# Kernel tuning notes

Measured on AMD Instinct MI355X. Metric: run time of the kernel, lower is better.

## Reference

```python
import jax, jax.numpy as jnp
import numpy as np

DIM = 256
HEADS = 8
HEAD_DIM = DIM // HEADS


def setup_inputs() -> dict:
    key = jax.random.key(0)
    ks = jax.random.split(key, 10)
    B, Nq, Nk, C = 2, 2048, 2048, DIM
    inp = {
        "query": jax.random.normal(ks[0], (B, Nq, C), jnp.float32),
        "key": jax.random.normal(ks[1], (B, Nk, C), jnp.float32),
        "value": jax.random.normal(ks[2], (B, Nk, C), jnp.float32),
        "qpos": jnp.zeros((B, Nq), jnp.int32),
        "kpos": jnp.zeros((B, Nk), jnp.int32),
        "mask": jax.random.randint(ks[3], (Nq, Nk), 0, 2) > 0,
        "similarities": jax.random.normal(ks[4], (B, HEADS, Nq, Nk), jnp.float32),
        # learned params (torch Linear stored here as [C_in, C_out]; no qkv bias)
        "Wq": jax.random.normal(ks[5], (C, C), jnp.float32) / np.sqrt(C),
        "Wk": jax.random.normal(ks[6], (C, C), jnp.float32) / np.sqrt(C),
        "Wv": jax.random.normal(ks[7], (C, C), jnp.float32) / np.sqrt(C),
        "Wp": jax.random.normal(ks[8], (C, C), jnp.float32) / np.sqrt(C),
        "bp": jax.random.normal(ks[9], (C,), jnp.float32) * 0.01,
    }
    return inp


def reference(query, key, value, qpos, kpos, mask, similarities, Wq, Wk, Wv, Wp, bp):
    B, Nq, C = query.shape
    Nk = key.shape[1]
    H, hd = HEADS, HEAD_DIM
    scale = hd ** -0.5
    # projections -> [B, N, H, hd] (rope is None, so qpos/kpos are unused)
    q = (query @ Wq).reshape(B, Nq, H, hd)
    k = (key @ Wk).reshape(B, Nk, H, hd)
    v = (value @ Wv).reshape(B, Nk, H, hd)
    # scores [B, H, Nq, Nk]
    attn = jnp.einsum("bqhd,bkhd->bhqk", q, k) * scale
    # mean-centered similarity bias (mean over heads, dim=1)
    attn = attn + (similarities - similarities.mean(axis=1, keepdims=True))
    # boolean mask: fill False positions with -inf, then softmax over keys
    attn = jnp.where(mask[None, None, :, :], attn, -jnp.inf)
    attn = jax.nn.softmax(attn, axis=-1)
    # AV -> [B, Nq, C], output projection
    x = jnp.einsum("bhqk,bkhd->bqhd", attn, v).reshape(B, Nq, C)
    return x @ Wp + bp
```

## Files before the change

kernel.cpp:

```cpp
#include <hip/hip_runtime.h>

#define B_  2
#define NQ  2048
#define NK  2048
#define C_  256
#define H_  8
#define HD  32
#define SPLIT 4
#define KSEG (NK / SPLIT)
#define KT   (KSEG / 32)
#define QT_  (NQ / 16)
#define PART_STRIDE 544

typedef float f32x4 __attribute__((ext_vector_type(4)));
typedef __bf16 bf16x8 __attribute__((ext_vector_type(8)));
typedef unsigned short ushort8 __attribute__((ext_vector_type(8)));

static __device__ __forceinline__ unsigned short f2bf(float f) {
    unsigned int u = __builtin_bit_cast(unsigned int, f);
    u += 0x7FFFu + ((u >> 16) & 1u);
    return (unsigned short)(u >> 16);
}
static __device__ __forceinline__ float bf2f(unsigned short h) {
    unsigned int u = ((unsigned int)h) << 16;
    return __builtin_bit_cast(float, u);
}
static __device__ __forceinline__ unsigned int split1(float f) {
    unsigned short h = f2bf(f);
    unsigned short l = f2bf(f - bf2f(h));
    return (unsigned int)h | ((unsigned int)l << 16);
}
static __device__ __forceinline__ bf16x8 ld_bf16x8(const unsigned short* p) {
    return __builtin_bit_cast(bf16x8, *(const ushort8*)p);
}
static __device__ __forceinline__ void async16(const void* g, void* l) {
    __builtin_amdgcn_global_load_lds((__attribute__((address_space(1))) void*)g,
                                     (__attribute__((address_space(3))) void*)l,
                                     16, 0, 0);
}

__global__ __launch_bounds__(256) void proj_kernel(
        const float* __restrict__ query, const float* __restrict__ key,
        const float* __restrict__ value,
        const float* __restrict__ Wq, const float* __restrict__ Wk,
        const float* __restrict__ Wv,
        unsigned short* __restrict__ qbh, unsigned short* __restrict__ qbl,
        unsigned short* __restrict__ kbh, unsigned short* __restrict__ kbl,
        unsigned short* __restrict__ vbh, unsigned short* __restrict__ vbl)
{
    __shared__ unsigned short WtH[64][32];
    __shared__ unsigned short WtL[64][32];

    const int z = blockIdx.z;
    const float* X = (z == 0) ? query : (z == 1) ? key : value;
    const float* W = (z == 0) ? Wq    : (z == 1) ? Wk  : Wv;
    unsigned short* dh = (z == 0) ? qbh : (z == 1) ? kbh : vbh;
    unsigned short* dl = (z == 0) ? qbl : (z == 1) ? kbl : vbl;
    const int vmode = (z == 2);

    const int tid  = threadIdx.x;
    const int wave = tid >> 6;
    const int lane = tid & 63;
    const int n15  = lane & 15;
    const int quad = lane >> 4;
    const int m0   = blockIdx.x * 64;
    const int j0   = blockIdx.y * 64;

    f32x4 acc[4];
    acc[0] = 0.f; acc[1] = 0.f; acc[2] = 0.f; acc[3] = 0.f;

    const int sj  = tid >> 2;
    const int skc = (tid & 3) * 8;
    const float* __restrict__ xrow = X + (size_t)(m0 + wave * 16 + n15) * C_;

    for (int k0 = 0; k0 < C_; k0 += 32) {
        ushort8 wh, wl;
        #pragma unroll
        for (int i = 0; i < 8; ++i) {
            unsigned int p = split1(W[(size_t)(k0 + skc + i) * C_ + j0 + sj]);
            wh[i] = (unsigned short)p;
            wl[i] = (unsigned short)(p >> 16);
        }
        *(ushort8*)&WtH[sj][skc] = wh;
        *(ushort8*)&WtL[sj][skc] = wl;
        __syncthreads();

        f32x4 a0 = *(const f32x4*)(xrow + k0 + quad * 8);
        f32x4 a1 = *(const f32x4*)(xrow + k0 + quad * 8 + 4);
        ushort8 ah, al;
        #pragma unroll
        for (int i = 0; i < 4; ++i) {
            unsigned int p0 = split1(a0[i]);
            unsigned int p1 = split1(a1[i]);
            ah[i]     = (unsigned short)p0;  al[i]     = (unsigned short)(p0 >> 16);
            ah[i + 4] = (unsigned short)p1;  al[i + 4] = (unsigned short)(p1 >> 16);
        }
        bf16x8 Ah = __builtin_bit_cast(bf16x8, ah);
        bf16x8 Al = __builtin_bit_cast(bf16x8, al);

        #pragma unroll
        for (int f = 0; f < 4; ++f) {
            bf16x8 Bh = ld_bf16x8(&WtH[f * 16 + n15][quad * 8]);
            bf16x8 Bl = ld_bf16x8(&WtL[f * 16 + n15][quad * 8]);
            acc[f] = __builtin_amdgcn_mfma_f32_16x16x32_bf16(Al, Bl, acc[f], 0, 0, 0);
            acc[f] = __builtin_amdgcn_mfma_f32_16x16x32_bf16(Al, Bh, acc[f], 0, 0, 0);
            acc[f] = __builtin_amdgcn_mfma_f32_16x16x32_bf16(Ah, Bl, acc[f], 0, 0, 0);
            acc[f] = __builtin_amdgcn_mfma_f32_16x16x32_bf16(Ah, Bh, acc[f], 0, 0, 0);
        }
        __syncthreads();
    }

    #pragma unroll
    for (int f = 0; f < 4; ++f) {
        const int j = j0 + f * 16 + n15;
        const int h = j >> 5, dd = j & 31;
        #pragma unroll
        for (int r = 0; r < 4; ++r) {
            const int grow = m0 + wave * 16 + quad * 4 + r;
            const int b = grow >> 11, row = grow & 2047;
            unsigned int p = split1(acc[f][r]);
            size_t idx;
            if (vmode) idx = (size_t)((b * H_ + h) * HD + dd) * NK + row;
            else       idx = (size_t)((b * H_ + h) * NK + row) * HD + dd;
            dh[idx] = (unsigned short)p;
            dl[idx] = (unsigned short)(p >> 16);
        }
    }
}

__global__ __launch_bounds__(256) void outproj_kernel(const unsigned short* __restrict__ Xh,
                                                      const unsigned short* __restrict__ Xl,
                                                      const float* __restrict__ W,
                                                      const float* __restrict__ bias,
                                                      float* __restrict__ out)
{
    __shared__ unsigned short WtH[64][32];
    __shared__ unsigned short WtL[64][32];

    const int tid  = threadIdx.x;
    const int wave = tid >> 6;
    const int lane = tid & 63;
    const int n15  = lane & 15;
    const int quad = lane >> 4;
    const int m0   = blockIdx.x * 64;
    const int j0   = blockIdx.y * 64;

    f32x4 acc[4];
    acc[0] = 0.f; acc[1] = 0.f; acc[2] = 0.f; acc[3] = 0.f;

    const int sj  = tid >> 2;
    const int skc = (tid & 3) * 8;
    const size_t xoff = (size_t)(m0 + wave * 16 + n15) * C_;

    for (int k0 = 0; k0 < C_; k0 += 32) {
        ushort8 wh, wl;
        #pragma unroll
        for (int i = 0; i < 8; ++i) {
            unsigned int p = split1(W[(size_t)(k0 + skc + i) * C_ + j0 + sj]);
            wh[i] = (unsigned short)p;
            wl[i] = (unsigned short)(p >> 16);
        }
        *(ushort8*)&WtH[sj][skc] = wh;
        *(ushort8*)&WtL[sj][skc] = wl;
        __syncthreads();

        bf16x8 Ah = ld_bf16x8(Xh + xoff + k0 + quad * 8);
        bf16x8 Al = ld_bf16x8(Xl + xoff + k0 + quad * 8);

        #pragma unroll
        for (int f = 0; f < 4; ++f) {
            bf16x8 Bh = ld_bf16x8(&WtH[f * 16 + n15][quad * 8]);
            bf16x8 Bl = ld_bf16x8(&WtL[f * 16 + n15][quad * 8]);
            acc[f] = __builtin_amdgcn_mfma_f32_16x16x32_bf16(Al, Bl, acc[f], 0, 0, 0);
            acc[f] = __builtin_amdgcn_mfma_f32_16x16x32_bf16(Al, Bh, acc[f], 0, 0, 0);
            acc[f] = __builtin_amdgcn_mfma_f32_16x16x32_bf16(Ah, Bl, acc[f], 0, 0, 0);
            acc[f] = __builtin_amdgcn_mfma_f32_16x16x32_bf16(Ah, Bh, acc[f], 0, 0, 0);
        }
        __syncthreads();
    }

    #pragma unroll
    for (int f = 0; f < 4; ++f) {
        const int j = j0 + f * 16 + n15;
        const float bj = bias[j];
        #pragma unroll
        for (int r = 0; r < 4; ++r) {
            const int grow = m0 + wave * 16 + quad * 4 + r;
            out[(size_t)grow * C_ + j] = acc[f][r] + bj;
        }
    }
}

__global__ __launch_bounds__(512, 6) void attn_kernel(
        const unsigned short* __restrict__ qh, const unsigned short* __restrict__ ql,
        const unsigned short* __restrict__ kh, const unsigned short* __restrict__ kl,
        const unsigned short* __restrict__ vh, const unsigned short* __restrict__ vl,
        const float* __restrict__ sim, const int* __restrict__ mask,
        float* __restrict__ part)
{
    __shared__ float simLds[2][H_][16][32];
    __shared__ int   maskLds[2][16][32];
    __shared__ float biasLds[16][33];
    __shared__ __align__(16) unsigned short pLds[H_][16 * 40];

    const int tid  = threadIdx.x;
    const int wave = tid >> 6;
    const int lane = tid & 63;
    const int n15  = lane & 15;
    const int quad = lane >> 4;

    const int wg   = blockIdx.x;
    const int s    = wg >> 8;
    const int rem  = wg & 255;
    const int b    = rem >> 7;
    const int qt   = rem & 127;
    const int q0   = qt * 16;
    const int kbeg = s * KSEG;

    const size_t bh   = (size_t)(b * H_ + wave);
    const size_t qoff = (bh * NQ + q0 + n15) * HD + quad * 8;
    const unsigned short* khb = kh + bh * NK * HD;
    const unsigned short* klb = kl + bh * NK * HD;
    const unsigned short* vhb = vh + bh * HD * NK;
    const unsigned short* vlb = vl + bh * HD * NK;
    const float* gsim = sim + (bh * NQ + q0) * (size_t)NK + kbeg
                            + (size_t)(lane >> 3) * NK + (lane & 7) * 4;
    const int* gmask = mask + (size_t)(q0 + (lane >> 3)) * NK + kbeg + (lane & 7) * 4;

    const bf16x8 Qh = ld_bf16x8(qh + qoff);
    const bf16x8 Ql = ld_bf16x8(ql + qoff);

    f32x4 O0 = 0.f, O1 = 0.f;
    float m_r[4] = {0.f, 0.f, 0.f, 0.f};
    float l_r[4] = {0.f, 0.f, 0.f, 0.f};

    async16(gsim,                  &simLds[0][wave][0][0]);
    async16(gsim + (size_t)8 * NK, &simLds[0][wave][8][0]);
    if (wave == 0) {
        async16(gmask,                  &maskLds[0][0][0]);
        async16(gmask + (size_t)8 * NK, &maskLds[0][8][0]);
    }

    const float scale = 0.17677669529663687f;

    for (int it = 0; it < KT; ++it) {
        const int k0  = kbeg + it * 32;
        const int cur = it & 1;

        __syncthreads();

        {
            const int qq = tid >> 5, kk = tid & 31;
            float sum = 0.f;
            #pragma unroll
            for (int h = 0; h < H_; ++h) sum += simLds[cur][h][qq][kk];
            biasLds[qq][kk] = maskLds[cur][qq][kk] ? (-0.125f * sum) : -1e30f;
        }
        __syncthreads();

        if (it + 1 < KT) {
            const float* g  = gsim + it * 32 + 32;
            async16(g,                  &simLds[cur ^ 1][wave][0][0]);
            async16(g + (size_t)8 * NK, &simLds[cur ^ 1][wave][8][0]);
            if (wave == 0) {
                const int* gm = gmask + it * 32 + 32;
                async16(gm,                  &maskLds[cur ^ 1][0][0]);
                async16(gm + (size_t)8 * NK, &maskLds[cur ^ 1][8][0]);
            }
        }

        const size_t koA = (size_t)(k0 + n15) * HD + quad * 8;
        const size_t koB = (size_t)(k0 + 16 + n15) * HD + quad * 8;
        bf16x8 Kh0 = ld_bf16x8(khb + koA), Kl0 = ld_bf16x8(klb + koA);
        bf16x8 Kh1 = ld_bf16x8(khb + koB), Kl1 = ld_bf16x8(klb + koB);

        f32x4 S0 = 0.f, S1 = 0.f;
        S0 = __builtin_amdgcn_mfma_f32_16x16x32_bf16(Ql, Kl0, S0, 0, 0, 0);
        S0 = __builtin_amdgcn_mfma_f32_16x16x32_bf16(Ql, Kh0, S0, 0, 0, 0);
        S0 = __builtin_amdgcn_mfma_f32_16x16x32_bf16(Qh, Kl0, S0, 0, 0, 0);
        S0 = __builtin_amdgcn_mfma_f32_16x16x32_bf16(Qh, Kh0, S0, 0, 0, 0);
        S1 = __builtin_amdgcn_mfma_f32_16x16x32_bf16(Ql, Kl1, S1, 0, 0, 0);
        S1 = __builtin_amdgcn_mfma_f32_16x16x32_bf16(Ql, Kh1, S1, 0, 0, 0);
        S1 = __builtin_amdgcn_mfma_f32_16x16x32_bf16(Qh, Kl1, S1, 0, 0, 0);
        S1 = __builtin_amdgcn_mfma_f32_16x16x32_bf16(Qh, Kh1, S1, 0, 0, 0);

        const size_t voA = (size_t)n15 * NK + k0 + quad * 8;
        const size_t voB = (size_t)(16 + n15) * NK + k0 + quad * 8;
        bf16x8 Vh0 = ld_bf16x8(vhb + voA), Vl0 = ld_bf16x8(vlb + voA);
        bf16x8 Vh1 = ld_bf16x8(vhb + voB), Vl1 = ld_bf16x8(vlb + voB);

        unsigned int u0[4], u1[4];
        #pragma unroll
        for (int r = 0; r < 4; ++r) {
            const int qq = quad * 4 + r;
            float s0 = S0[r] * scale + simLds[cur][wave][qq][n15]      + biasLds[qq][n15];
            float s1 = S1[r] * scale + simLds[cur][wave][qq][16 + n15] + biasLds[qq][16 + n15];

            float mx = fmaxf(s0, s1);
            #pragma unroll
            for (int off = 1; off < 16; off <<= 1) mx = fmaxf(mx, __shfl_xor(mx, off));
            const float mnew = fmaxf(m_r[r], mx);
            const float a  = __expf(m_r[r] - mnew);
            const float p0 = __expf(s0 - mnew);
            const float p1 = __expf(s1 - mnew);
            float sm = p0 + p1;
            #pragma unroll
            for (int off = 1; off < 16; off <<= 1) sm += __shfl_xor(sm, off);
            l_r[r] = l_r[r] * a + sm;
            m_r[r] = mnew;
            O0[r] *= a; O1[r] *= a;
            u0[r] = split1(p0); u1[r] = split1(p1);
        }

        unsigned short* pw = pLds[wave];
        #pragma unroll
        for (int r = 0; r < 4; ++r) {
            const int qq = quad * 4 + r;
            pw[qq * 40 + n15]      = (unsigned short)u0[r];
            pw[qq * 40 + 16 + n15] = (unsigned short)u1[r];
        }
        bf16x8 Ph = ld_bf16x8(pw + n15 * 40 + quad * 8);
        #pragma unroll
        for (int r = 0; r < 4; ++r) {
            const int qq = quad * 4 + r;
            pw[qq * 40 + n15]      = (unsigned short)(u0[r] >> 16);
            pw[qq * 40 + 16 + n15] = (unsigned short)(u1[r] >> 16);
        }
        bf16x8 Pl = ld_bf16x8(pw + n15 * 40 + quad * 8);

        O0 = __builtin_amdgcn_mfma_f32_16x16x32_bf16(Pl, Vl0, O0, 0, 0, 0);
        O0 = __builtin_amdgcn_mfma_f32_16x16x32_bf16(Pl, Vh0, O0, 0, 0, 0);
        O0 = __builtin_amdgcn_mfma_f32_16x16x32_bf16(Ph, Vl0, O0, 0, 0, 0);
        O0 = __builtin_amdgcn_mfma_f32_16x16x32_bf16(Ph, Vh0, O0, 0, 0, 0);
        O1 = __builtin_amdgcn_mfma_f32_16x16x32_bf16(Pl, Vl1, O1, 0, 0, 0);
        O1 = __builtin_amdgcn_mfma_f32_16x16x32_bf16(Pl, Vh1, O1, 0, 0, 0);
        O1 = __builtin_amdgcn_mfma_f32_16x16x32_bf16(Ph, Vl1, O1, 0, 0, 0);
        O1 = __builtin_amdgcn_mfma_f32_16x16x32_bf16(Ph, Vh1, O1, 0, 0, 0);
    }

    float* pb = part + (size_t)(((s * B_ + b) * H_ + wave) * QT_ + qt) * PART_STRIDE;
    #pragma unroll
    for (int r = 0; r < 4; ++r) {
        const int q = quad * 4 + r;
        pb[q * 32 + n15]      = O0[r];
        pb[q * 32 + 16 + n15] = O1[r];
        if (n15 == 0) {
            pb[512 + q] = m_r[r];
            pb[528 + q] = l_r[r];
        }
    }
}

__global__ __launch_bounds__(256) void combine_kernel(const float* __restrict__ part,
                                                      unsigned short* __restrict__ xh,
                                                      unsigned short* __restrict__ xl)
{
    const int wid  = blockIdx.x * 4 + (threadIdx.x >> 6);
    const int lane = threadIdx.x & 63;
    const int b  = wid >> 10;
    const int h  = (wid >> 7) & 7;
    const int qt = wid & 127;
    const int q  = lane >> 2;
    const int d0 = (lane & 3) * 8;

    float ms[SPLIT], ls[SPLIT];
    float mstar = -1e30f;
    #pragma unroll
    for (int s = 0; s < SPLIT; ++s) {
        const float* pb = part + (size_t)(((s * B_ + b) * H_ + h) * QT_ + qt) * PART_STRIDE;
        ms[s] = pb[512 + q];
        ls[s] = pb[528 + q];
        mstar = fmaxf(mstar, ms[s]);
    }
    f32x4 acc0 = 0.f, acc1 = 0.f;
    float lsum = 0.f;
    #pragma unroll
    for (int s = 0; s < SPLIT; ++s) {
        const float* pb = part + (size_t)(((s * B_ + b) * H_ + h) * QT_ + qt) * PART_STRIDE;
        const float w = __expf(ms[s] - mstar);
        lsum += w * ls[s];
        f32x4 o0 = *(const f32x4*)(pb + q * 32 + d0);
        f32x4 o1 = *(const f32x4*)(pb + q * 32 + d0 + 4);
        acc0 += w * o0;
        acc1 += w * o1;
    }
    const float inv = 1.0f / lsum;
    const size_t base = (size_t)(b * NQ + qt * 16 + q) * C_ + h * HD + d0;
    #pragma unroll
    for (int i = 0; i < 4; ++i) {
        unsigned int p0 = split1(acc0[i] * inv);
        unsigned int p1 = split1(acc1[i] * inv);
        xh[base + i]     = (unsigned short)p0;
        xl[base + i]     = (unsigned short)(p0 >> 16);
        xh[base + 4 + i] = (unsigned short)p1;
        xl[base + 4 + i] = (unsigned short)(p1 >> 16);
    }
}

extern "C" void kernel_launch(void* const* d_in, const int* in_sizes, int n_in,
                              void* d_out, int out_size, void* d_ws, size_t ws_size,
                              hipStream_t stream) {
    const float* query = (const float*)d_in[0];
    const float* key   = (const float*)d_in[1];
    const float* value = (const float*)d_in[2];
    const int*   mask  = (const int*)d_in[5];
    const float* sim   = (const float*)d_in[6];
    const float* Wq  = (const float*)d_in[7];
    const float* Wk  = (const float*)d_in[8];
    const float* Wv  = (const float*)d_in[9];
    const float* Wp  = (const float*)d_in[10];
    const float* bp  = (const float*)d_in[11];
    float* out = (float*)d_out;

    const size_t NEL = (size_t)B_ * H_ * NQ * HD;
    unsigned short* qbh = (unsigned short*)d_ws;
    unsigned short* qbl = qbh + NEL;
    unsigned short* kbh = qbl + NEL;
    unsigned short* kbl = kbh + NEL;
    unsigned short* vbh = kbl + NEL;
    unsigned short* vbl = vbh + NEL;
    unsigned short* xbh = vbl + NEL;
    unsigned short* xbl = xbh + NEL;
    float* part = (float*)(xbl + NEL);

    proj_kernel<<<dim3(64, 4, 3), 256, 0, stream>>>(query, key, value, Wq, Wk, Wv,
                                                    qbh, qbl, kbh, kbl, vbh, vbl);
    attn_kernel<<<SPLIT * 256, 512, 0, stream>>>(qbh, qbl, kbh, kbl, vbh, vbl,
                                                 sim, mask, part);
    combine_kernel<<<512, 256, 0, stream>>>(part, xbh, xbl);
    outproj_kernel<<<dim3(64, 4), 256, 0, stream>>>(xbh, xbl, Wp, bp, out);
}
```

Before: 568.3 us.

## Drop split-K attention, process key chunks of 128 with register prefetch and bitpacked mask

Removes the split-K decomposition and combine kernel so each workgroup covers all keys for a query tile and writes the normalized output directly. The key loop now processes four 32-key tiles per barrier pair, with K/V and mask loaded into registers and the next similarity chunk fetched asynchronously into LDS. The int mask is first packed into 16-bit per-column bitmasks by a new kernel. Weight LDS tiles in the projection kernels are padded to reduce bank conflicts. The grid shrinks to 256 workgroups of 512 threads, which may underfill the GPU's compute units, and register pressure rises.

Result: no change. 565.6 us (-0.5%).

```diff
diff --git a/kernel.cpp b/kernel.cpp
--- a/kernel.cpp
+++ b/kernel.cpp
@@ -6,11 +6,11 @@
 #define C_  256
 #define H_  8
 #define HD  32
-#define SPLIT 4
-#define KSEG (NK / SPLIT)
-#define KT   (KSEG / 32)
+#define KT   (NK / 32)
+#define CH   4
+#define NC   (KT / CH)
+#define CCOLS (CH * 32)
 #define QT_  (NQ / 16)
-#define PART_STRIDE 544
 
 typedef float f32x4 __attribute__((ext_vector_type(4)));
 typedef __bf16 bf16x8 __attribute__((ext_vector_type(8)));
@@ -37,6 +37,18 @@
     __builtin_amdgcn_global_load_lds((__attribute__((address_space(1))) void*)g,
                                      (__attribute__((address_space(3))) void*)l,
                                      16, 0, 0);
+}
+
+__global__ __launch_bounds__(256) void maskpack_kernel(const int* __restrict__ mask,
+                                                       unsigned short* __restrict__ mb)
+{
+    const int qt = blockIdx.x;
+    const int k  = blockIdx.y * 256 + threadIdx.x;
+    unsigned int m = 0;
+    #pragma unroll
+    for (int r = 0; r < 16; ++r)
+        m |= (mask[(size_t)(qt * 16 + r) * NK + k] ? 1u : 0u) << r;
+    mb[(size_t)qt * NK + k] = (unsigned short)m;
 }
 
 __global__ __launch_bounds__(256) void proj_kernel(
@@ -48,8 +60,8 @@
         unsigned short* __restrict__ kbh, unsigned short* __restrict__ kbl,
         unsigned short* __restrict__ vbh, unsigned short* __restrict__ vbl)
 {
-    __shared__ unsigned short WtH[64][32];
-    __shared__ unsigned short WtL[64][32];
+    __shared__ unsigned short WtH[64][40];
+    __shared__ unsigned short WtL[64][40];
 
     const int z = blockIdx.z;
     const float* X = (z == 0) ? query : (z == 1) ? key : value;
@@ -134,8 +146,8 @@
                                                       const float* __restrict__ bias,
                                                       float* __restrict__ out)
 {
-    __shared__ unsigned short WtH[64][32];
-    __shared__ unsigned short WtL[64][32];
+    __shared__ unsigned short WtH[64][40];
+    __shared__ unsigned short WtL[64][40];
 
     const int tid  = threadIdx.x;
     const int wave = tid >> 6;
@@ -191,16 +203,15 @@
     }
 }
 
-__global__ __launch_bounds__(512, 6) void attn_kernel(
+__global__ __launch_bounds__(512, 2) void attn_kernel(
         const unsigned short* __restrict__ qh, const unsigned short* __restrict__ ql,
         const unsigned short* __restrict__ kh, const unsigned short* __restrict__ kl,
         const unsigned short* __restrict__ vh, const unsigned short* __restrict__ vl,
-        const float* __restrict__ sim, const int* __restrict__ mask,
-        float* __restrict__ part)
+        const float* __restrict__ sim, const unsigned short* __restrict__ maskb,
+        unsigned short* __restrict__ xh, unsigned short* __restrict__ xl)
 {
-    __shared__ float simLds[2][H_][16][32];
-    __shared__ int   maskLds[2][16][32];
-    __shared__ float biasLds[16][33];
+    __shared__ __align__(16) float simC[2][H_][16][CCOLS];
+    __shared__ float hsum[16][CCOLS];
     __shared__ __align__(16) unsigned short pLds[H_][16 * 40];
 
     const int tid  = threadIdx.x;
@@ -209,13 +220,10 @@
     const int n15  = lane & 15;
     const int quad = lane >> 4;
 
-    const int wg   = blockIdx.x;
-    const int s    = wg >> 8;
-    const int rem  = wg & 255;
-    const int b    = rem >> 7;
-    const int qt   = rem & 127;
-    const int q0   = qt * 16;
-    const int kbeg = s * KSEG;
+    const int wg = blockIdx.x;
+    const int b  = wg >> 7;
+    const int qt = wg & 127;
+    const int q0 = qt * 16;
 
     const size_t bh   = (size_t)(b * H_ + wave);
     const size_t qoff = (bh * NQ + q0 + n15) * HD + quad * 8;
@@ -223,9 +231,9 @@
     const unsigned short* klb = kl + bh * NK * HD;
     const unsigned short* vhb = vh + bh * HD * NK;
     const unsigned short* vlb = vl + bh * HD * NK;
-    const float* gsim = sim + (bh * NQ + q0) * (size_t)NK + kbeg
-                            + (size_t)(lane >> 3) * NK + (lane & 7) * 4;
-    const int* gmask = mask + (size_t)(q0 + (lane >> 3)) * NK + kbeg + (lane & 7) * 4;
+    const unsigned short* mkb = maskb + (size_t)qt * NK;
+    const float* gsim = sim + (bh * NQ + q0 + (lane >> 5)) * (size_t)NK
+                            + (lane & 31) * 4;
 
     const bf16x8 Qh = ld_bf16x8(qh + qoff);
     const bf16x8 Ql = ld_bf16x8(ql + qoff);
@@ -234,166 +242,149 @@
     float m_r[4] = {0.f, 0.f, 0.f, 0.f};
     float l_r[4] = {0.f, 0.f, 0.f, 0.f};
 
-    async16(gsim,                  &simLds[0][wave][0][0]);
-    async16(gsim + (size_t)8 * NK, &simLds[0][wave][8][0]);
-    if (wave == 0) {
-        async16(gmask,                  &maskLds[0][0][0]);
-        async16(gmask + (size_t)8 * NK, &maskLds[0][8][0]);
-    }
-
     const float scale = 0.17677669529663687f;
 
-    for (int it = 0; it < KT; ++it) {
-        const int k0  = kbeg + it * 32;
-        const int cur = it & 1;
-
-        __syncthreads();
-
-        {
-            const int qq = tid >> 5, kk = tid & 31;
+    auto fetch_chunk = [&](int c, int buf) {
+        const float* g = gsim + (size_t)c * CCOLS;
+        #pragma unroll
+        for (int ci = 0; ci < 8; ++ci)
+            async16(g + (size_t)(2 * ci) * NK, &simC[buf][wave][2 * ci][0]);
+    };
+
+    auto headsum_phase = [&](int cur) {
+        const int qq = tid >> 5, kk = tid & 31;
+        #pragma unroll
+        for (int j = 0; j < 4; ++j) {
             float sum = 0.f;
             #pragma unroll
-            for (int h = 0; h < H_; ++h) sum += simLds[cur][h][qq][kk];
-            biasLds[qq][kk] = maskLds[cur][qq][kk] ? (-0.125f * sum) : -1e30f;
-        }
-        __syncthreads();
-
-        if (it + 1 < KT) {
-            const float* g  = gsim + it * 32 + 32;
-            async16(g,                  &simLds[cur ^ 1][wave][0][0]);
-            async16(g + (size_t)8 * NK, &simLds[cur ^ 1][wave][8][0]);
-            if (wave == 0) {
-                const int* gm = gmask + it * 32 + 32;
-                async16(gm,                  &maskLds[cur ^ 1][0][0]);
-                async16(gm + (size_t)8 * NK, &maskLds[cur ^ 1][8][0]);
+            for (int h = 0; h < H_; ++h) sum += simC[cur][h][qq][kk + 32 * j];
+            hsum[qq][kk + 32 * j] = -0.125f * sum;
+        }
+    };
+
+    struct KVT {
+        bf16x8 kh[CH][2], kl[CH][2], vh[CH][2], vl[CH][2];
+        unsigned short mb[CH][2];
+    };
+
+    auto load_kv = [&](int c, KVT& kv) {
+        #pragma unroll
+        for (int t = 0; t < CH; ++t) {
+            const int k0 = c * CCOLS + t * 32;
+            const size_t koA = (size_t)(k0 + n15) * HD + quad * 8;
+            const size_t koB = (size_t)(k0 + 16 + n15) * HD + quad * 8;
+            kv.kh[t][0] = ld_bf16x8(khb + koA); kv.kl[t][0] = ld_bf16x8(klb + koA);
+            kv.kh[t][1] = ld_bf16x8(khb + koB); kv.kl[t][1] = ld_bf16x8(klb + koB);
+            const size_t voA = (size_t)n15 * NK + k0 + quad * 8;
+            const size_t voB = (size_t)(16 + n15) * NK + k0 + quad * 8;
+            kv.vh[t][0] = ld_bf16x8(vhb + voA); kv.vl[t][0] = ld_bf16x8(vlb + voA);
+            kv.vh[t][1] = ld_bf16x8(vhb + voB); kv.vl[t][1] = ld_bf16x8(vlb + voB);
+            kv.mb[t][0] = mkb[k0 + n15];
+            kv.mb[t][1] = mkb[k0 + 16 + n15];
+        }
+    };
+
+    auto chunk_body = [&](int cur, const KVT& kv) {
+        unsigned short* pw = pLds[wave];
+        #pragma unroll
+        for (int t = 0; t < CH; ++t) {
+            const int tc = t * 32;
+            f32x4 S0 = 0.f, S1 = 0.f;
+            S0 = __builtin_amdgcn_mfma_f32_16x16x32_bf16(Ql, kv.kl[t][0], S0, 0, 0, 0);
+            S0 = __builtin_amdgcn_mfma_f32_16x16x32_bf16(Ql, kv.kh[t][0], S0, 0, 0, 0);
+            S0 = __builtin_amdgcn_mfma_f32_16x16x32_bf16(Qh, kv.kl[t][0], S0, 0, 0, 0);
+            S0 = __builtin_amdgcn_mfma_f32_16x16x32_bf16(Qh, kv.kh[t][0], S0, 0, 0, 0);
+            S1 = __builtin_amdgcn_mfma_f32_16x16x32_bf16(Ql, kv.kl[t][1], S1, 0, 0, 0);
+            S1 = __builtin_amdgcn_mfma_f32_16x16x32_bf16(Ql, kv.kh[t][1], S1, 0, 0, 0);
+            S1 = __builtin_amdgcn_mfma_f32_16x16x32_bf16(Qh, kv.kl[t][1], S1, 0, 0, 0);
+            S1 = __builtin_amdgcn_mfma_f32_16x16x32_bf16(Qh, kv.kh[t][1], S1, 0, 0, 0);
+
+            unsigned int u0[4], u1[4];
+            #pragma unroll
+            for (int r = 0; r < 4; ++r) {
+                const int qq = quad * 4 + r;
+                float s0 = S0[r] * scale + simC[cur][wave][qq][tc + n15]
+                         + hsum[qq][tc + n15];
+                float s1 = S1[r] * scale + simC[cur][wave][qq][tc + 16 + n15]
+                         + hsum[qq][tc + 16 + n15];
+                if (!((kv.mb[t][0] >> qq) & 1)) s0 = -1e30f;
+                if (!((kv.mb[t][1] >> qq) & 1)) s1 = -1e30f;
+
+                float mx = fmaxf(s0, s1);
+                #pragma unroll
+                for (int off = 1; off < 16; off <<= 1) mx = fmaxf(mx, __shfl_xor(mx, off));
+                const float mnew = fmaxf(m_r[r], mx);
+                const float a  = __expf(m_r[r] - mnew);
+                const float p0 = __expf(s0 - mnew);
+                const float p1 = __expf(s1 - mnew);
+                float sm = p0 + p1;
+                #pragma unroll
+                for (int off = 1; off < 16; off <<= 1) sm += __shfl_xor(sm, off);
+                l_r[r] = l_r[r] * a + sm;
+                m_r[r] = mnew;
+                O0[r] *= a; O1[r] *= a;
+                u0[r] = split1(p0); u1[r] = split1(p1);
             }
-        }
-
-        const size_t koA = (size_t)(k0 + n15) * HD + quad * 8;
-        const size_t koB = (size_t)(k0 + 16 + n15) * HD + quad * 8;
-        bf16x8 Kh0 = ld_bf16x8(khb + koA), Kl0 = ld_bf16x8(klb + koA);
-        bf16x8 Kh1 = ld_bf16x8(khb + koB), Kl1 = ld_bf16x8(klb + koB);
-
-        f32x4 S0 = 0.f, S1 = 0.f;
-        S0 = __builtin_amdgcn_mfma_f32_16x16x32_bf16(Ql, Kl0, S0, 0, 0, 0);
-        S0 = __builtin_amdgcn_mfma_f32_16x16x32_bf16(Ql, Kh0, S0, 0, 0, 0);
-        S0 = __builtin_amdgcn_mfma_f32_16x16x32_bf16(Qh, Kl0, S0, 0, 0, 0);
-        S0 = __builtin_amdgcn_mfma_f32_16x16x32_bf16(Qh, Kh0, S0, 0, 0, 0);
-        S1 = __builtin_amdgcn_mfma_f32_16x16x32_bf16(Ql, Kl1, S1, 0, 0, 0);
-        S1 = __builtin_amdgcn_mfma_f32_16x16x32_bf16(Ql, Kh1, S1, 0, 0, 0);
-        S1 = __builtin_amdgcn_mfma_f32_16x16x32_bf16(Qh, Kl1, S1, 0, 0, 0);
-        S1 = __builtin_amdgcn_mfma_f32_16x16x32_bf16(Qh, Kh1, S1, 0, 0, 0);
-
-        const size_t voA = (size_t)n15 * NK + k0 + quad * 8;
-        const size_t voB = (size_t)(16 + n15) * NK + k0 + quad * 8;
-        bf16x8 Vh0 = ld_bf16x8(vhb + voA), Vl0 = ld_bf16x8(vlb + voA);
-        bf16x8 Vh1 = ld_bf16x8(vhb + voB), Vl1 = ld_bf16x8(vlb + voB);
-
-        unsigned int u0[4], u1[4];
-        #pragma unroll
-        for (int r = 0; r < 4; ++r) {
-            const int qq = quad * 4 + r;
-            float s0 = S0[r] * scale + simLds[cur][wave][qq][n15]      + biasLds[qq][n15];
-            float s1 = S1[r] * scale + simLds[cur][wave][qq][16 + n15] + biasLds[qq][16 + n15];
-
-            float mx = fmaxf(s0, s1);
+
             #pragma unroll
-            for (int off = 1; off < 16; off <<= 1) mx = fmaxf(mx, __shfl_xor(mx, off));
-            const float mnew = fmaxf(m_r[r], mx);
-            const float a  = __expf(m_r[r] - mnew);
-            const float p0 = __expf(s0 - mnew);
-            const float p1 = __expf(s1 - mnew);
-            float sm = p0 + p1;
+            for (int r = 0; r < 4; ++r) {
+                const int qq = quad * 4 + r;
+                pw[qq * 40 + n15]      = (unsigned short)u0[r];
+                pw[qq * 40 + 16 + n15] = (unsigned short)u1[r];
+            }
+            bf16x8 Ph = ld_bf16x8(pw + n15 * 40 + quad * 8);
             #pragma unroll
-            for (int off = 1; off < 16; off <<= 1) sm += __shfl_xor(sm, off);
-            l_r[r] = l_r[r] * a + sm;
-            m_r[r] = mnew;
-            O0[r] *= a; O1[r] *= a;
-            u0[r] = split1(p0); u1[r] = split1(p1);
-        }
-
-        unsigned short* pw = pLds[wave];
-        #pragma unroll
-        for (int r = 0; r < 4; ++r) {
-            const int qq = quad * 4 + r;
-            pw[qq * 40 + n15]      = (unsigned short)u0[r];
-            pw[qq * 40 + 16 + n15] = (unsigned short)u1[r];
-        }
-        bf16x8 Ph = ld_bf16x8(pw + n15 * 40 + quad * 8);
-        #pragma unroll
-        for (int r = 0; r < 4; ++r) {
-            const int qq = quad * 4 + r;
-            pw[qq * 40 + n15]      = (unsigned short)(u0[r] >> 16);
-            pw[qq * 40 + 16 + n15] = (unsigned short)(u1[r] >> 16);
-        }
-        bf16x8 Pl = ld_bf16x8(pw + n15 * 40 + quad * 8);
-
-        O0 = __builtin_amdgcn_mfma_f32_16x16x32_bf16(Pl, Vl0, O0, 0, 0, 0);
-        O0 = __builtin_amdgcn_mfma_f32_16x16x32_bf16(Pl, Vh0, O0, 0, 0, 0);
-        O0 = __builtin_amdgcn_mfma_f32_16x16x32_bf16(Ph, Vl0, O0, 0, 0, 0);
-        O0 = __builtin_amdgcn_mfma_f32_16x16x32_bf16(Ph, Vh0, O0, 0, 0, 0);
-        O1 = __builtin_amdgcn_mfma_f32_16x16x32_bf16(Pl, Vl1, O1, 0, 0, 0);
-        O1 = __builtin_amdgcn_mfma_f32_16x16x32_bf16(Pl, Vh1, O1, 0, 0, 0);
-        O1 = __builtin_amdgcn_mfma_f32_16x16x32_bf16(Ph, Vl1, O1, 0, 0, 0);
-        O1 = __builtin_amdgcn_mfma_f32_16x16x32_bf16(Ph, Vh1, O1, 0, 0, 0);
-    }
-
-    float* pb = part + (size_t)(((s * B_ + b) * H_ + wave) * QT_ + qt) * PART_STRIDE;
+            for (int r = 0; r < 4; ++r) {
+                const int qq = quad * 4 + r;
+                pw[qq * 40 + n15]      = (unsigned short)(u0[r] >> 16);
+                pw[qq * 40 + 16 + n15] = (unsigned short)(u1[r] >> 16);
+            }
+            bf16x8 Pl = ld_bf16x8(pw + n15 * 40 + quad * 8);
+
+            O0 = __builtin_amdgcn_mfma_f32_16x16x32_bf16(Pl, kv.vl[t][0], O0, 0, 0, 0);
+            O0 = __builtin_amdgcn_mfma_f32_16x16x32_bf16(Pl, kv.vh[t][0], O0, 0, 0, 0);
+            O0 = __builtin_amdgcn_mfma_f32_16x16x32_bf16(Ph, kv.vl[t][0], O0, 0, 0, 0);
+            O0 = __builtin_amdgcn_mfma_f32_16x16x32_bf16(Ph, kv.vh[t][0], O0, 0, 0, 0);
+            O1 = __builtin_amdgcn_mfma_f32_16x16x32_bf16(Pl, kv.vl[t][1], O1, 0, 0, 0);
+            O1 = __builtin_amdgcn_mfma_f32_16x16x32_bf16(Pl, kv.vh[t][1], O1, 0, 0, 0);
+            O1 = __builtin_amdgcn_mfma_f32_16x16x32_bf16(Ph, kv.vl[t][1], O1, 0, 0, 0);
+            O1 = __builtin_amdgcn_mfma_f32_16x16x32_bf16(Ph, kv.vh[t][1], O1, 0, 0, 0);
+        }
+    };
+
+    fetch_chunk(0, 0);
+    KVT kv;
+    for (int c = 0; c < NC - 1; ++c) {
+        const int cur = c & 1;
+        __syncthreads();
+        headsum_phase(cur);
+        __syncthreads();
+        load_kv(c, kv);
+        __builtin_amdgcn_sched_barrier(0);
+        fetch_chunk(c + 1, cur ^ 1);
+        __builtin_amdgcn_sched_barrier(0);
+        chunk_body(cur, kv);
+    }
+    {
+        const int cur = (NC - 1) & 1;
+        __syncthreads();
+        headsum_phase(cur);
+        __syncthreads();
+        load_kv(NC - 1, kv);
+        chunk_body(cur, kv);
+    }
+
     #pragma unroll
     for (int r = 0; r < 4; ++r) {
         const int q = quad * 4 + r;
-        pb[q * 32 + n15]      = O0[r];
-        pb[q * 32 + 16 + n15] = O1[r];
-        if (n15 == 0) {
-            pb[512 + q] = m_r[r];
-            pb[528 + q] = l_r[r];
-        }
-    }
-}
-
-__global__ __launch_bounds__(256) void combine_kernel(const float* __restrict__ part,
-                                                      unsigned short* __restrict__ xh,
-                                                      unsigned short* __restrict__ xl)
-{
-    const int wid  = blockIdx.x * 4 + (threadIdx.x >> 6);
-    const int lane = threadIdx.x & 63;
-    const int b  = wid >> 10;
-    const int h  = (wid >> 7) & 7;
-    const int qt = wid & 127;
-    const int q  = lane >> 2;
-    const int d0 = (lane & 3) * 8;
-
-    float ms[SPLIT], ls[SPLIT];
-    float mstar = -1e30f;
-    #pragma unroll
-    for (int s = 0; s < SPLIT; ++s) {
-        const float* pb = part + (size_t)(((s * B_ + b) * H_ + h) * QT_ + qt) * PART_STRIDE;
-        ms[s] = pb[512 + q];
-        ls[s] = pb[528 + q];
-        mstar = fmaxf(mstar, ms[s]);
-    }
-    f32x4 acc0 = 0.f, acc1 = 0.f;
-    float lsum = 0.f;
-    #pragma unroll
-    for (int s = 0; s < SPLIT; ++s) {
-        const float* pb = part + (size_t)(((s * B_ + b) * H_ + h) * QT_ + qt) * PART_STRIDE;
-        const float w = __expf(ms[s] - mstar);
-        lsum += w * ls[s];
-        f32x4 o0 = *(const f32x4*)(pb + q * 32 + d0);
-        f32x4 o1 = *(const f32x4*)(pb + q * 32 + d0 + 4);
-        acc0 += w * o0;
-        acc1 += w * o1;
-    }
-    const float inv = 1.0f / lsum;
-    const size_t base = (size_t)(b * NQ + qt * 16 + q) * C_ + h * HD + d0;
-    #pragma unroll
-    for (int i = 0; i < 4; ++i) {
-        unsigned int p0 = split1(acc0[i] * inv);
-        unsigned int p1 = split1(acc1[i] * inv);
-        xh[base + i]     = (unsigned short)p0;
-        xl[base + i]     = (unsigned short)(p0 >> 16);
-        xh[base + 4 + i] = (unsigned short)p1;
-        xl[base + 4 + i] = (unsigned short)(p1 >> 16);
+        const float inv = 1.0f / l_r[r];
+        const size_t base = (size_t)(b * NQ + q0 + q) * C_ + wave * HD;
+        unsigned int p0 = split1(O0[r] * inv);
+        unsigned int p1 = split1(O1[r] * inv);
+        xh[base + n15]      = (unsigned short)p0;
+        xl[base + n15]      = (unsigned short)(p0 >> 16);
+        xh[base + 16 + n15] = (unsigned short)p1;
+        xl[base + 16 + n15] = (unsigned short)(p1 >> 16);
     }
 }
 
@@ -421,12 +412,12 @@
     unsigned short* vbl = vbh + NEL;
     unsigned short* xbh = vbl + NEL;
     unsigned short* xbl = xbh + NEL;
-    float* part = (float*)(xbl + NEL);
-
+    unsigned short* maskbW = xbl + NEL;
+
+    maskpack_kernel<<<dim3(QT_, NK / 256), 256, 0, stream>>>(mask, maskbW);
     proj_kernel<<<dim3(64, 4, 3), 256, 0, stream>>>(query, key, value, Wq, Wk, Wv,
                                                     qbh, qbl, kbh, kbl, vbh, vbl);
-    attn_kernel<<<SPLIT * 256, 512, 0, stream>>>(qbh, qbl, kbh, kbl, vbh, vbl,
-                                                 sim, mask, part);
-    combine_kernel<<<512, 256, 0, stream>>>(part, xbh, xbl);
+    attn_kernel<<<B_ * QT_, 512, 0, stream>>>(qbh, qbl, kbh, kbl, vbh, vbl,
+                                              sim, maskbW, xbh, xbl);
     outproj_kernel<<<dim3(64, 4), 256, 0, stream>>>(xbh, xbl, Wp, bp, out);
 }
```

## Bit-pack mask per query tile, pad weight LDS, and reorder attention prefetch loads

Applied to the files above, without the earlier changes.

A new pre-pass kernel packs the int mask into 16-bit words, one per key column per 16-row query tile. The attention kernel then reads one short per thread per key tile into a register instead of async-copying the int mask through LDS. The V loads and the next-tile sim prefetch are moved earlier, ahead of the QK MFMAs, with scheduling barriers so global latency overlaps compute. The weight LDS tiles in the projection kernels are padded from 32 to 40 columns to reduce bank conflicts. The cost is an extra kernel launch and more workspace memory.

Result: slower. 643.2 us (+13.2%).

```diff
diff --git a/kernel.cpp b/kernel.cpp
--- a/kernel.cpp
+++ b/kernel.cpp
@@ -39,6 +39,18 @@
                                      16, 0, 0);
 }
 
+__global__ __launch_bounds__(256) void maskpack_kernel(const int* __restrict__ mask,
+                                                       unsigned short* __restrict__ mb)
+{
+    const int qt = blockIdx.x;
+    const int k  = blockIdx.y * 256 + threadIdx.x;
+    unsigned int m = 0;
+    #pragma unroll
+    for (int r = 0; r < 16; ++r)
+        m |= (mask[(size_t)(qt * 16 + r) * NK + k] ? 1u : 0u) << r;
+    mb[(size_t)qt * NK + k] = (unsigned short)m;
+}
+
 __global__ __launch_bounds__(256) void proj_kernel(
         const float* __restrict__ query, const float* __restrict__ key,
         const float* __restrict__ value,
@@ -48,8 +60,8 @@
         unsigned short* __restrict__ kbh, unsigned short* __restrict__ kbl,
         unsigned short* __restrict__ vbh, unsigned short* __restrict__ vbl)
 {
-    __shared__ unsigned short WtH[64][32];
-    __shared__ unsigned short WtL[64][32];
+    __shared__ unsigned short WtH[64][40];
+    __shared__ unsigned short WtL[64][40];
 
     const int z = blockIdx.z;
     const float* X = (z == 0) ? query : (z == 1) ? key : value;
@@ -134,8 +146,8 @@
                                                       const float* __restrict__ bias,
                                                       float* __restrict__ out)
 {
-    __shared__ unsigned short WtH[64][32];
-    __shared__ unsigned short WtL[64][32];
+    __shared__ unsigned short WtH[64][40];
+    __shared__ unsigned short WtL[64][40];
 
     const int tid  = threadIdx.x;
     const int wave = tid >> 6;
@@ -195,11 +207,10 @@
         const unsigned short* __restrict__ qh, const unsigned short* __restrict__ ql,
         const unsigned short* __restrict__ kh, const unsigned short* __restrict__ kl,
         const unsigned short* __restrict__ vh, const unsigned short* __restrict__ vl,
-        const float* __restrict__ sim, const int* __restrict__ mask,
+        const float* __restrict__ sim, const unsigned short* __restrict__ maskb,
         float* __restrict__ part)
 {
-    __shared__ float simLds[2][H_][16][32];
-    __shared__ int   maskLds[2][16][32];
+    __shared__ __align__(16) float simLds[2][H_][16][32];
     __shared__ float biasLds[16][33];
     __shared__ __align__(16) unsigned short pLds[H_][16 * 40];
 
@@ -223,9 +234,9 @@
     const unsigned short* klb = kl + bh * NK * HD;
     const unsigned short* vhb = vh + bh * HD * NK;
     const unsigned short* vlb = vl + bh * HD * NK;
-    const float* gsim = sim + (bh * NQ + q0) * (size_t)NK + kbeg
-                            + (size_t)(lane >> 3) * NK + (lane & 7) * 4;
-    const int* gmask = mask + (size_t)(q0 + (lane >> 3)) * NK + kbeg + (lane & 7) * 4;
+    const unsigned short* mkb = maskb + (size_t)qt * NK + kbeg;
+    const float* gsim = sim + (bh * NQ + q0 + (lane >> 3)) * (size_t)NK + kbeg
+                            + (lane & 7) * 4;
 
     const bf16x8 Qh = ld_bf16x8(qh + qoff);
     const bf16x8 Ql = ld_bf16x8(ql + qoff);
@@ -234,45 +245,46 @@
     float m_r[4] = {0.f, 0.f, 0.f, 0.f};
     float l_r[4] = {0.f, 0.f, 0.f, 0.f};
 
+    const float scale = 0.17677669529663687f;
+    const int kk = tid & 31;
+
     async16(gsim,                  &simLds[0][wave][0][0]);
     async16(gsim + (size_t)8 * NK, &simLds[0][wave][8][0]);
-    if (wave == 0) {
-        async16(gmask,                  &maskLds[0][0][0]);
-        async16(gmask + (size_t)8 * NK, &maskLds[0][8][0]);
-    }
-
-    const float scale = 0.17677669529663687f;
+    unsigned short mcur = mkb[kk];
 
     for (int it = 0; it < KT; ++it) {
         const int k0  = kbeg + it * 32;
         const int cur = it & 1;
+        const int last = (it == KT - 1);
 
         __syncthreads();
 
         {
-            const int qq = tid >> 5, kk = tid & 31;
+            const int qq = tid >> 5;
             float sum = 0.f;
             #pragma unroll
             for (int h = 0; h < H_; ++h) sum += simLds[cur][h][qq][kk];
-            biasLds[qq][kk] = maskLds[cur][qq][kk] ? (-0.125f * sum) : -1e30f;
-        }
-        __syncthreads();
-
-        if (it + 1 < KT) {
-            const float* g  = gsim + it * 32 + 32;
-            async16(g,                  &simLds[cur ^ 1][wave][0][0]);
-            async16(g + (size_t)8 * NK, &simLds[cur ^ 1][wave][8][0]);
-            if (wave == 0) {
-                const int* gm = gmask + it * 32 + 32;
-                async16(gm,                  &maskLds[cur ^ 1][0][0]);
-                async16(gm + (size_t)8 * NK, &maskLds[cur ^ 1][8][0]);
-            }
-        }
+            biasLds[qq][kk] = ((mcur >> qq) & 1) ? (-0.125f * sum) : -1e30f;
+        }
+        __syncthreads();
 
         const size_t koA = (size_t)(k0 + n15) * HD + quad * 8;
         const size_t koB = (size_t)(k0 + 16 + n15) * HD + quad * 8;
         bf16x8 Kh0 = ld_bf16x8(khb + koA), Kl0 = ld_bf16x8(klb + koA);
         bf16x8 Kh1 = ld_bf16x8(khb + koB), Kl1 = ld_bf16x8(klb + koB);
+        const size_t voA = (size_t)n15 * NK + k0 + quad * 8;
+        const size_t voB = (size_t)(16 + n15) * NK + k0 + quad * 8;
+        bf16x8 Vh0 = ld_bf16x8(vhb + voA), Vl0 = ld_bf16x8(vlb + voA);
+        bf16x8 Vh1 = ld_bf16x8(vhb + voB), Vl1 = ld_bf16x8(vlb + voB);
+        if (!last) mcur = mkb[(it + 1) * 32 + kk];
+
+        if (!last) {
+            __builtin_amdgcn_sched_barrier(0);
+            const float* g = gsim + it * 32 + 32;
+            async16(g,                  &simLds[cur ^ 1][wave][0][0]);
+            async16(g + (size_t)8 * NK, &simLds[cur ^ 1][wave][8][0]);
+            __builtin_amdgcn_sched_barrier(0);
+        }
 
         f32x4 S0 = 0.f, S1 = 0.f;
         S0 = __builtin_amdgcn_mfma_f32_16x16x32_bf16(Ql, Kl0, S0, 0, 0, 0);
@@ -283,11 +295,6 @@
         S1 = __builtin_amdgcn_mfma_f32_16x16x32_bf16(Ql, Kh1, S1, 0, 0, 0);
         S1 = __builtin_amdgcn_mfma_f32_16x16x32_bf16(Qh, Kl1, S1, 0, 0, 0);
         S1 = __builtin_amdgcn_mfma_f32_16x16x32_bf16(Qh, Kh1, S1, 0, 0, 0);
-
-        const size_t voA = (size_t)n15 * NK + k0 + quad * 8;
-        const size_t voB = (size_t)(16 + n15) * NK + k0 + quad * 8;
-        bf16x8 Vh0 = ld_bf16x8(vhb + voA), Vl0 = ld_bf16x8(vlb + voA);
-        bf16x8 Vh1 = ld_bf16x8(vhb + voB), Vl1 = ld_bf16x8(vlb + voB);
 
         unsigned int u0[4], u1[4];
         #pragma unroll
@@ -422,11 +429,14 @@
     unsigned short* xbh = vbl + NEL;
     unsigned short* xbl = xbh + NEL;
     float* part = (float*)(xbl + NEL);
-
+    unsigned short* maskbW = (unsigned short*)(part
+                            + (size_t)SPLIT * B_ * H_ * QT_ * PART_STRIDE);
+
+    maskpack_kernel<<<dim3(QT_, NK / 256), 256, 0, stream>>>(mask, maskbW);
     proj_kernel<<<dim3(64, 4, 3), 256, 0, stream>>>(query, key, value, Wq, Wk, Wv,
                                                     qbh, qbl, kbh, kbl, vbh, vbl);
     attn_kernel<<<SPLIT * 256, 512, 0, stream>>>(qbh, qbl, kbh, kbl, vbh, vbl,
-                                                 sim, mask, part);
+                                                 sim, maskbW, part);
     combine_kernel<<<512, 256, 0, stream>>>(part, xbh, xbl);
     outproj_kernel<<<dim3(64, 4), 256, 0, stream>>>(xbh, xbl, Wp, bp, out);
 }
```
